# Kernel optimization log

Measured on AMD Instinct MI355X. Metric: run time of the kernel, lower is better.

Reference implementation:

```python
import jax, jax.numpy as jnp
import numpy as np

N = 50000      # nodes
E = 800000     # edges (avg degree 16)
RAW = 128      # raw_dim
HID = 256      # hidden_dim
OUT = 64       # out_dim
K = 4          # n_kernels
PHI = 16       # phi_dim
EPS = 1e-8


def setup_inputs() -> dict:
    key = jax.random.key(0)
    ks = jax.random.split(key, 8)
    h_l = jax.random.normal(ks[0], (N, HID), jnp.float32)
    e_l = jax.random.normal(ks[1], (N, RAW), jnp.float32)
    src = jax.random.randint(ks[2], (E,), 0, N, dtype=jnp.int32)
    dst = jax.random.randint(ks[3], (E,), 0, N, dtype=jnp.int32)
    gain = np.sqrt(2.0)
    W_phi = jax.random.normal(ks[4], (RAW, PHI - 1), jnp.float32) * (gain * np.sqrt(2.0 / (RAW + PHI - 1)))
    W1 = jax.random.normal(ks[5], (HID, RAW), jnp.float32) * np.sqrt(2.0 / (RAW + HID))
    b1 = jnp.zeros((HID,), jnp.float32)
    W2 = jax.random.normal(ks[6], (K * PHI, HID), jnp.float32) * np.sqrt(2.0 / (HID + K * PHI))
    b2 = jnp.zeros((K * PHI,), jnp.float32)
    tilde_phi = jnp.eye(PHI, dtype=jnp.float32)[-K:]       # n_kernels <= phi_dim branch
    W = jax.random.normal(ks[7], (HID, OUT * K), jnp.float32) * (gain * np.sqrt(2.0 / (HID + OUT * K)))
    bias = jnp.zeros((OUT,), jnp.float32)
    return {"h_l": h_l, "e_l": e_l, "src": src, "dst": dst,
            "W_phi": W_phi, "W1": W1, "b1": b1, "W2": W2, "b2": b2,
            "tilde_phi": tilde_phi, "W": W, "bias": bias}


def reference(h_l, e_l, src, dst, W_phi, W1, b1, W2, b2, tilde_phi, W, bias):
    # per-node kernelized features: [N, K, OUT]
    h = (h_l @ W).reshape(N, K, OUT)
    # pseudo-coordinates: [N, PHI-1]
    phi_k = e_l @ W_phi
    # normalized kernel anchors: [K, PHI]
    tilde_norm = tilde_phi / jnp.linalg.norm(tilde_phi, axis=1, keepdims=True)
    # deformation offsets: [N, K, PHI]
    hid = jax.nn.relu(e_l @ W1.T + b1)
    delta_k = (hid @ W2.T + b2).reshape(N, K, PHI)
    delta_ik = tilde_norm[None, :, :] + delta_k            # [N, K, PHI]

    # edge relative position (u_sub_v): [E, PHI-1]
    dist = phi_k[src] - phi_k[dst]
    mask = jnp.all(dist == 0.0, axis=1)                    # self/coincident edges
    dist = jnp.concatenate([dist, mask.astype(dist.dtype)[:, None]], axis=1)  # [E, PHI]
    dist = dist / jnp.clip(jnp.linalg.norm(dist, axis=1, keepdims=True), EPS)

    # per-edge per-kernel attention logit: a_ijk = <dist, delta_ik[dst]>  -> [E, K]
    a = jnp.einsum('ep,ekp->ek', dist, delta_ik[dst])

    # edge_softmax: softmax over incoming edges per destination node
    m = jax.ops.segment_max(a, dst, num_segments=N)        # [N, K]
    ex = jnp.exp(a - m[dst])
    s = jax.ops.segment_sum(ex, dst, num_segments=N)       # [N, K]
    att = ex / s[dst]                                      # [E, K]

    # message passing: u_mul_e then sum over incoming edges
    msg = h[src] * att[:, :, None]                         # [E, K, OUT]
    agg = jax.ops.segment_sum(msg, dst, num_segments=N)    # [N, K, OUT]

    out = agg.sum(axis=1) + bias[None, :]                  # [N, OUT]
    out = out / jnp.clip(jnp.linalg.norm(out, axis=1, keepdims=True), EPS)

    # regularizers
    d2 = ((tilde_norm[:, None, :] - tilde_norm[None, :, :]) ** 2).sum(-1)  # [K, K]
    l_sep = d2.sum() / K                                   # sum_k mean_j ||.||^2
    l_focus = (delta_k ** 2).sum(-1).mean()
    return out, l_sep, l_focus
```

## Files before the change

### kernel.cpp

```cpp
#include <hip/hip_runtime.h>
#include <math.h>

#define NN 50000
#define EE 800000

typedef __attribute__((ext_vector_type(8))) short short8;
typedef __attribute__((ext_vector_type(4))) float f32x4;
typedef __attribute__((ext_vector_type(2))) float f32x2;

__device__ inline unsigned short f2b(float f) {
    unsigned u = __float_as_uint(f);
    unsigned r = (u + 0x7FFFu + ((u >> 16) & 1u)) >> 16;
    return (unsigned short)r;
}
__device__ inline unsigned char f2fp8(float v) {
    return (unsigned char)(__builtin_amdgcn_cvt_pk_fp8_f32(v, v, 0, false) & 0xFF);
}
__device__ inline unsigned cvt_pk_bf16(float lo, float hi) {
    unsigned r;
    asm("v_cvt_pk_bf16_f32 %0, %1, %2" : "=v"(r) : "v"(lo), "v"(hi));
    return r;
}
__device__ inline void gload16(const unsigned short* g, unsigned short* l) {
    __builtin_amdgcn_global_load_lds(
        (const __attribute__((address_space(1))) void*)g,
        (__attribute__((address_space(3))) void*)l, 16, 0, 0);
}

#define PREP_THREADS (800000 + 65536 + 32768 + 16384 + 2048)

__global__ __launch_bounds__(256) void prep_k(const float* __restrict__ W,
                                              const float* __restrict__ W1,
                                              const float* __restrict__ W2,
                                              const float* __restrict__ W_phi,
                                              const float* __restrict__ tilde_phi,
                                              const int* __restrict__ dst,
                                              unsigned short* __restrict__ W_t,
                                              unsigned short* __restrict__ W1_bf,
                                              unsigned short* __restrict__ W2_bf,
                                              unsigned short* __restrict__ Wphi_t,
                                              int* __restrict__ deg,
                                              int* __restrict__ rank,
                                              float* __restrict__ tnorm,
                                              float* __restrict__ lsep_out) {
    if (blockIdx.x == 0) {
        __shared__ float tn[64];
        int t = threadIdx.x;
        if (t < 64) {
            float v = tilde_phi[t];
            float sq = v * v;
            #pragma unroll
            for (int s = 8; s; s >>= 1) sq += __shfl_xor(sq, s, 16);
            float tnv = v / sqrtf(sq);
            tn[t] = tnv;
            tnorm[t] = tnv;
        }
        __syncthreads();
        if (t == 0) {
            float tot = 0.f;
            for (int a = 0; a < 4; ++a)
                for (int b = 0; b < 4; ++b) {
                    float s2 = 0.f;
                    for (int p = 0; p < 16; ++p) {
                        float df = tn[a * 16 + p] - tn[b * 16 + p];
                        s2 += df * df;
                    }
                    tot += s2;
                }
            lsep_out[0] = tot * 0.25f;
        }
    }
    int i = blockIdx.x * 256 + threadIdx.x;
    if (i < 800000) {
        rank[i] = atomicAdd(&deg[dst[i]], 1);
    } else if (i < 865536) {
        int j = i - 800000;
        int cp = j >> 8, r = j & 255;
        int ch = cp >> 2, k = cp & 3;
        W_t[j] = f2b(W[(size_t)r * 256 + (k << 6) + ch]);
    } else if (i < 898304) {
        int j = i - 865536;
        W1_bf[j] = f2b(W1[j]);
    } else if (i < 914688) {
        int j = i - 898304;
        W2_bf[j] = f2b(W2[j]);
    } else if (i < 916736) {
        int j = i - 914688;
        int cp = j >> 7, r = j & 127;
        Wphi_t[j] = (cp < 15) ? f2b(W_phi[(size_t)r * 15 + cp]) : (unsigned short)0;
    }
}

template <int KD, int BM, int BN, int WR, int WC, bool RELU, int OMODE,
          bool AF32, bool LFOCUS, bool TNADJ>
__device__ __forceinline__ void ggemm_body(unsigned short* lds,
                                           const void* __restrict__ A,
                                           const unsigned short* __restrict__ Bt,
                                           const float* __restrict__ bias_vec,
                                           void* __restrict__ Cout, int ldc,
                                           float* __restrict__ lfocus_part,
                                           const float* __restrict__ tn_vec,
                                           int bxm, int bxn) {
    const int AM = BM / (WR * 16), AN = BN / (WC * 16);
    unsigned short* As = lds;
    unsigned short* Bs = lds + BM * 32;
    const int tid = threadIdx.x;
    const int l = tid & 63, l15 = l & 15, l4 = l >> 4;
    const int w = tid >> 6;
    const int wr = w / WC, wc = w % WC;
    const int row0 = bxm * BM;
    const int col0 = bxn * BN;
    const int wrow = wr * AM * 16, wcol = wc * AN * 16;

    auto stage = [&](int k0) {
        #pragma unroll
        for (int o = tid; o < BM * 4; o += 256) {
            int r = o >> 2, s = o & 3;
            int gr = row0 + r; if (gr >= NN) gr = NN - 1;
            if (AF32) {
                const float* Af = (const float*)A + (size_t)gr * KD + k0 + s * 8;
                float4 f0 = *(const float4*)Af;
                float4 f1 = *(const float4*)(Af + 4);
                *(uint4*)&As[o * 8] = make_uint4(cvt_pk_bf16(f0.x, f0.y),
                                                 cvt_pk_bf16(f0.z, f0.w),
                                                 cvt_pk_bf16(f1.x, f1.y),
                                                 cvt_pk_bf16(f1.z, f1.w));
            } else {
                gload16(&((const unsigned short*)A)[(size_t)gr * KD + k0 + s * 8],
                        &As[(o - l) * 8]);
            }
        }
        #pragma unroll
        for (int o = tid; o < BN * 4; o += 256) {
            int r = o >> 2, s = o & 3;
            gload16(&Bt[(size_t)(col0 + r) * KD + k0 + s * 8], &Bs[(o - l) * 8]);
        }
    };

    f32x4 acc[AM][AN];
    #pragma unroll
    for (int m = 0; m < AM; ++m)
        #pragma unroll
        for (int n = 0; n < AN; ++n)
            acc[m][n] = (f32x4){0.f, 0.f, 0.f, 0.f};

    const int NT = KD / 32;
    stage(0);
    for (int t = 0; t < NT; ++t) {
        __syncthreads();
        short8 af[AM], bfr[AN];
        #pragma unroll
        for (int m = 0; m < AM; ++m)
            af[m] = *(const short8*)&As[((wrow + m * 16 + l15) * 4 + l4) * 8];
        #pragma unroll
        for (int n = 0; n < AN; ++n)
            bfr[n] = *(const short8*)&Bs[((wcol + n * 16 + l15) * 4 + l4) * 8];
        #pragma unroll
        for (int m = 0; m < AM; ++m)
            #pragma unroll
            for (int n = 0; n < AN; ++n)
                acc[m][n] = __builtin_amdgcn_mfma_f32_16x16x32_bf16(af[m], bfr[n], acc[m][n], 0, 0, 0);
        if (t + 1 < NT) {
            __syncthreads();
            stage((t + 1) * 32);
        }
    }

    float lf = 0.f;
    #pragma unroll
    for (int m = 0; m < AM; ++m) {
        #pragma unroll
        for (int n = 0; n < AN; ++n) {
            int gc = col0 + wcol + n * 16 + l15;
            float bv = bias_vec ? bias_vec[gc] : 0.f;
            float tv = TNADJ ? tn_vec[gc] : 0.f;
            #pragma unroll
            for (int r = 0; r < 4; ++r) {
                int gr = row0 + wrow + m * 16 + l4 * 4 + r;
                if (gr >= NN) continue;
                float v = acc[m][n][r] + bv;
                if (RELU) v = fmaxf(v, 0.f);
                if (LFOCUS) lf += v * v;
                if (TNADJ) v += tv;
                if (OMODE == 0)
                    ((float*)Cout)[(size_t)gr * ldc + gc] = v;
                else if (OMODE == 1)
                    ((unsigned short*)Cout)[(size_t)gr * ldc + gc] = f2b(v);
                else
                    ((unsigned char*)Cout)[(size_t)gr * ldc + gc] = f2fp8(v);
            }
        }
    }
    if (LFOCUS) {
        #pragma unroll
        for (int s = 32; s; s >>= 1) lf += __shfl_xor(lf, s);
        __syncthreads();
        float* red = (float*)lds;
        if (l == 0) red[w] = lf;
        __syncthreads();
        if (tid == 0)
            lfocus_part[bxm] = red[0] + red[1] + red[2] + red[3];
    }
}

__global__ __launch_bounds__(256) void fused3_k(const float* __restrict__ e_l,
                                                const float* __restrict__ h_l,
                                                const unsigned short* __restrict__ W1_bf,
                                                const unsigned short* __restrict__ Wphi_t,
                                                const unsigned short* __restrict__ W_t,
                                                const float* __restrict__ b1,
                                                unsigned short* __restrict__ hid_bf,
                                                float* __restrict__ phi,
                                                unsigned char* __restrict__ h8,
                                                const int* __restrict__ src,
                                                const int* __restrict__ dst,
                                                const int* __restrict__ rank,
                                                const int* __restrict__ offs,
                                                int* __restrict__ csr_src) {
    __shared__ __align__(16) unsigned short lds[128 * 32 + 128 * 32];
    int bx = blockIdx.x;
    if (bx < 391) {
        int base = bx * 2048 + threadIdx.x;
        int pos[8], sv[8];
        #pragma unroll
        for (int j = 0; j < 8; ++j) {
            int e = base + j * 256;
            if (e < EE) {
                pos[j] = offs[dst[e]] + rank[e];
                sv[j] = src[e];
            } else pos[j] = -1;
        }
        #pragma unroll
        for (int j = 0; j < 8; ++j)
            if (pos[j] >= 0) csr_src[pos[j]] = sv[j];
    } else if (bx < 1173) {
        int b = bx - 391;
        ggemm_body<256, 128, 128, 2, 2, false, 2, true, false, false>(
            lds, h_l, W_t, nullptr, h8, 256, nullptr, nullptr, b >> 1, b & 1);
    } else if (bx < 1955) {
        int b = bx - 1173;
        ggemm_body<128, 128, 128, 2, 2, true, 1, true, false, false>(
            lds, e_l, W1_bf, b1, hid_bf, 256, nullptr, nullptr, b >> 1, b & 1);
    } else {
        ggemm_body<128, 128, 16, 4, 1, false, 0, true, false, false>(
            lds, e_l, Wphi_t, nullptr, phi, 16, nullptr, nullptr, bx - 1955, 0);
    }
}

__global__ __launch_bounds__(256) void delta_k(const unsigned short* __restrict__ hid_bf,
                                               const unsigned short* __restrict__ W2_bf,
                                               const float* __restrict__ b2,
                                               float* __restrict__ deltap,
                                               float* __restrict__ lfocus_part,
                                               const float* __restrict__ tnorm) {
    __shared__ __align__(16) unsigned short lds[32 * 32 + 64 * 32];
    ggemm_body<256, 32, 64, 1, 4, false, 0, false, true, true>(
        lds, hid_bf, W2_bf, b2, deltap, 64, lfocus_part, tnorm, blockIdx.x, 0);
}

#define SCAN_NB ((NN + 255) / 256)
#define DELTA_NB 1563

__global__ __launch_bounds__(256) void scan_partial_k(const int* __restrict__ deg,
                                                      int* __restrict__ bsum) {
    __shared__ int ws_[4];
    int i = blockIdx.x * 256 + threadIdx.x;
    int v = (i < NN) ? deg[i] : 0;
    int x = v;
    #pragma unroll
    for (int s = 32; s; s >>= 1) x += __shfl_xor(x, s);
    if ((threadIdx.x & 63) == 0) ws_[threadIdx.x >> 6] = x;
    __syncthreads();
    if (threadIdx.x == 0) bsum[blockIdx.x] = ws_[0] + ws_[1] + ws_[2] + ws_[3];
}

__global__ __launch_bounds__(256) void scan_bsum_k(int* __restrict__ bsum) {
    __shared__ int sd[256];
    int t = threadIdx.x;
    int v = (t < SCAN_NB) ? bsum[t] : 0;
    sd[t] = v;
    __syncthreads();
    for (int s = 1; s < 256; s <<= 1) {
        int u = (t >= s) ? sd[t - s] : 0;
        __syncthreads();
        sd[t] += u;
        __syncthreads();
    }
    if (t < SCAN_NB) bsum[t] = sd[t] - v;
}

__global__ __launch_bounds__(256) void scan_scatter_k(const int* __restrict__ deg,
                                                      const int* __restrict__ bsum,
                                                      int* __restrict__ offs,
                                                      int* __restrict__ csr_dst) {
    __shared__ int wexc[4];
    int i = blockIdx.x * 256 + threadIdx.x;
    int lane = threadIdx.x & 63, wid = threadIdx.x >> 6;
    int v = (i < NN) ? deg[i] : 0;
    int x = v;
    #pragma unroll
    for (int d = 1; d < 64; d <<= 1) { int u = __shfl_up(x, d); if (lane >= d) x += u; }
    if (lane == 63) wexc[wid] = x;
    __syncthreads();
    if (threadIdx.x == 0) {
        int a = wexc[0], b = wexc[1], c = wexc[2];
        wexc[0] = 0; wexc[1] = a; wexc[2] = a + b; wexc[3] = a + b + c;
    }
    __syncthreads();
    int excl = (x - v) + wexc[wid] + bsum[blockIdx.x];
    if (i < NN) {
        offs[i + 1] = excl + v;
        if (i == 0) offs[0] = 0;
        for (int q = excl; q < excl + v; ++q) csr_dst[q] = i;
    }
}

__global__ __launch_bounds__(256) void edge_w_k(const int* __restrict__ csr_src,
                                                const int* __restrict__ csr_dst,
                                                const float* __restrict__ phi,
                                                const float* __restrict__ deltap,
                                                float4* __restrict__ csr_w,
                                                const float* __restrict__ lfocus_part,
                                                float* __restrict__ lfocus_out) {
    if (blockIdx.x == 3125) {
        __shared__ float red[4];
        float s = 0.f;
        for (int i = threadIdx.x; i < DELTA_NB; i += 256) s += lfocus_part[i];
        #pragma unroll
        for (int st = 32; st; st >>= 1) s += __shfl_xor(s, st);
        if ((threadIdx.x & 63) == 0) red[threadIdx.x >> 6] = s;
        __syncthreads();
        if (threadIdx.x == 0)
            lfocus_out[0] = (red[0] + red[1] + red[2] + red[3]) * (1.f / ((float)NN * 4));
        return;
    }
    int e = blockIdx.x * 256 + threadIdx.x;
    if (e >= EE) return;
    int s = csr_src[e], d = csr_dst[e];
    const float4* ps4 = (const float4*)(phi + (size_t)s * 16);
    const float4* pd4 = (const float4*)(phi + (size_t)d * 16);
    float dv[16];
    float nrm2 = 0.f;
    #pragma unroll
    for (int q = 0; q < 4; ++q) {
        float4 a = ps4[q], b = pd4[q];
        dv[q * 4 + 0] = a.x - b.x;
        dv[q * 4 + 1] = a.y - b.y;
        dv[q * 4 + 2] = a.z - b.z;
        dv[q * 4 + 3] = a.w - b.w;
    }
    #pragma unroll
    for (int p = 0; p < 15; ++p) nrm2 += dv[p] * dv[p];
    float z = (nrm2 == 0.f) ? 1.f : 0.f;
    dv[15] = z;
    nrm2 += z;
    float inv = 1.f / fmaxf(sqrtf(nrm2), 1e-8f);
    const float* dl = deltap + (size_t)d * 64;
    float res[4];
    #pragma unroll
    for (int k = 0; k < 4; ++k) {
        const float4* dk = (const float4*)(dl + k * 16);
        float sacc = 0.f;
        #pragma unroll
        for (int q = 0; q < 4; ++q) {
            float4 tv = dk[q];
            sacc += dv[q * 4 + 0] * tv.x;
            sacc += dv[q * 4 + 1] * tv.y;
            sacc += dv[q * 4 + 2] * tv.z;
            sacc += dv[q * 4 + 3] * tv.w;
        }
        res[k] = sacc * inv;
    }
    csr_w[e] = make_float4(__expf(res[0]), __expf(res[1]),
                           __expf(res[2]), __expf(res[3]));
}

__global__ __launch_bounds__(256) void aggregate_k(const int* __restrict__ offs,
                                                   const int* __restrict__ csr_src,
                                                   const float* __restrict__ csr_wf,
                                                   const unsigned int* __restrict__ h8,
                                                   const float* __restrict__ bias,
                                                   float* __restrict__ out) {
    int wave = threadIdx.x >> 6;
    int lane = threadIdx.x & 63;
    int n = blockIdx.x * 4 + wave;
    if (n >= NN) return;
    int beg = offs[n], end = offs[n + 1];

    float part = 0.f;
    for (int q = beg * 4 + lane; q < end * 4; q += 64) part += csr_wf[q];
    #pragma unroll
    for (int s = 4; s < 64; s <<= 1) part += __shfl_xor(part, s);
    float inv = (part > 0.f) ? 1.f / part : 0.f;
    float i0 = __shfl(inv, 0), i1 = __shfl(inv, 1);
    float i2 = __shfl(inv, 2), i3 = __shfl(inv, 3);

    const float4* csr_w = (const float4*)csr_wf;
    float a0 = 0.f, a1 = 0.f, a2 = 0.f, a3 = 0.f;
    int p = beg;
    for (; p + 3 < end; p += 4) {
        float4 w0 = csr_w[p], w1 = csr_w[p + 1], w2 = csr_w[p + 2], w3 = csr_w[p + 3];
        int s0 = csr_src[p], s1 = csr_src[p + 1], s2 = csr_src[p + 2], s3 = csr_src[p + 3];
        unsigned hv0 = h8[(size_t)s0 * 64 + lane];
        unsigned hv1 = h8[(size_t)s1 * 64 + lane];
        unsigned hv2 = h8[(size_t)s2 * 64 + lane];
        unsigned hv3 = h8[(size_t)s3 * 64 + lane];
        f32x2 lo, hi;
        lo = __builtin_amdgcn_cvt_pk_f32_fp8(hv0, false);
        hi = __builtin_amdgcn_cvt_pk_f32_fp8(hv0, true);
        a0 += w0.x * lo.x; a1 += w0.y * lo.y; a2 += w0.z * hi.x; a3 += w0.w * hi.y;
        lo = __builtin_amdgcn_cvt_pk_f32_fp8(hv1, false);
        hi = __builtin_amdgcn_cvt_pk_f32_fp8(hv1, true);
        a0 += w1.x * lo.x; a1 += w1.y * lo.y; a2 += w1.z * hi.x; a3 += w1.w * hi.y;
        lo = __builtin_amdgcn_cvt_pk_f32_fp8(hv2, false);
        hi = __builtin_amdgcn_cvt_pk_f32_fp8(hv2, true);
        a0 += w2.x * lo.x; a1 += w2.y * lo.y; a2 += w2.z * hi.x; a3 += w2.w * hi.y;
        lo = __builtin_amdgcn_cvt_pk_f32_fp8(hv3, false);
        hi = __builtin_amdgcn_cvt_pk_f32_fp8(hv3, true);
        a0 += w3.x * lo.x; a1 += w3.y * lo.y; a2 += w3.z * hi.x; a3 += w3.w * hi.y;
    }
    for (; p < end; ++p) {
        float4 wA = csr_w[p];
        int sA = csr_src[p];
        unsigned hv = h8[(size_t)sA * 64 + lane];
        f32x2 lo = __builtin_amdgcn_cvt_pk_f32_fp8(hv, false);
        f32x2 hi = __builtin_amdgcn_cvt_pk_f32_fp8(hv, true);
        a0 += wA.x * lo.x; a1 += wA.y * lo.y; a2 += wA.z * hi.x; a3 += wA.w * hi.y;
    }
    float v = a0 * i0 + a1 * i1 + a2 * i2 + a3 * i3 + bias[lane];
    float nr = v * v;
    #pragma unroll
    for (int s = 32; s; s >>= 1) nr += __shfl_xor(nr, s);
    float invn = 1.f / fmaxf(sqrtf(nr), 1e-8f);
    out[(size_t)n * 64 + lane] = v * invn;
}

extern "C" void kernel_launch(void* const* d_in, const int* in_sizes, int n_in,
                              void* d_out, int out_size, void* d_ws, size_t ws_size,
                              hipStream_t stream) {
    const float* h_l       = (const float*)d_in[0];
    const float* e_l       = (const float*)d_in[1];
    const int*   src       = (const int*)d_in[2];
    const int*   dst       = (const int*)d_in[3];
    const float* W_phi     = (const float*)d_in[4];
    const float* W1        = (const float*)d_in[5];
    const float* b1        = (const float*)d_in[6];
    const float* W2        = (const float*)d_in[7];
    const float* b2        = (const float*)d_in[8];
    const float* tilde_phi = (const float*)d_in[9];
    const float* W         = (const float*)d_in[10];
    const float* bias      = (const float*)d_in[11];
    float* out = (float*)d_out;
    float* lsep_ptr   = out + (size_t)NN * 64;
    float* lfocus_ptr = out + (size_t)NN * 64 + 1;

    char* ws = (char*)d_ws;
    size_t off = 0;
    auto alloc = [&](size_t bytes) -> char* {
        char* p = ws + off;
        off += (bytes + 255) & ~(size_t)255;
        return p;
    };
    float*          phi     = (float*)alloc((size_t)NN * 16 * 4);
    float*          deltap  = (float*)alloc((size_t)NN * 64 * 4);
    unsigned char*  h8      = (unsigned char*)alloc((size_t)NN * 256);
    unsigned short* hid_bf  = (unsigned short*)alloc((size_t)NN * 256 * 2);
    int*            csr_src = (int*)alloc((size_t)EE * 4);
    int*            csr_dst = (int*)alloc((size_t)EE * 4);
    int*            rank    = (int*)alloc((size_t)EE * 4);
    float*          csr_w   = (float*)alloc((size_t)EE * 4 * 4);
    int*            deg     = (int*)alloc((size_t)NN * 4);
    int*            offs    = (int*)alloc((size_t)(NN + 1) * 4);
    int*            bsum    = (int*)alloc((size_t)SCAN_NB * 4);
    float*          lf_part = (float*)alloc((size_t)DELTA_NB * 4);
    unsigned short* W_t     = (unsigned short*)alloc(256 * 256 * 2);
    unsigned short* W1_bf   = (unsigned short*)alloc(256 * 128 * 2);
    unsigned short* W2_bf   = (unsigned short*)alloc(64 * 256 * 2);
    unsigned short* Wphi_t  = (unsigned short*)alloc(16 * 128 * 2);
    float*          tnorm   = (float*)alloc(64 * 4);

    hipMemsetAsync(deg, 0, (size_t)NN * 4, stream);

    prep_k<<<(PREP_THREADS + 255) / 256, 256, 0, stream>>>(
        W, W1, W2, W_phi, tilde_phi, dst,
        W_t, W1_bf, W2_bf, Wphi_t, deg, rank, tnorm, lsep_ptr);

    scan_partial_k<<<SCAN_NB, 256, 0, stream>>>(deg, bsum);
    scan_bsum_k<<<1, 256, 0, stream>>>(bsum);
    scan_scatter_k<<<SCAN_NB, 256, 0, stream>>>(deg, bsum, offs, csr_dst);

    fused3_k<<<2346, 256, 0, stream>>>(e_l, h_l, W1_bf, Wphi_t, W_t, b1,
                                       hid_bf, phi, h8, src, dst, rank, offs,
                                       csr_src);

    delta_k<<<DELTA_NB, 256, 0, stream>>>(hid_bf, W2_bf, b2, deltap, lf_part, tnorm);

    edge_w_k<<<3126, 256, 0, stream>>>(csr_src, csr_dst, phi, deltap, (float4*)csr_w,
                                       lf_part, lfocus_ptr);

    aggregate_k<<<12500, 256, 0, stream>>>(offs, csr_src, csr_w,
                                           (const unsigned int*)h8, bias, out);
}
```

Before: 178.9 us.

## Fuse hidden-layer GEMM, phi projection and delta GEMM into one block

The W1 GEMM, the W_phi projection and the W2 delta GEMM now run inside one fused block per 64-row tile. The ReLU hidden activations stay in padded LDS instead of being written to a global bf16 buffer and read back by a separate kernel. This removes the hidden-activation global round trip and one kernel launch, and the fused kernel moves to 512-thread blocks. In exchange it uses more LDS per block and gives the hidden and delta stage fewer, heavier blocks, which can lower occupancy.

```diff
diff --git a/kernel.cpp b/kernel.cpp
--- a/kernel.cpp
+++ b/kernel.cpp
@@ -91,175 +91,241 @@
     }
 }
 
-template <int KD, int BM, int BN, int WR, int WC, bool RELU, int OMODE,
-          bool AF32, bool LFOCUS, bool TNADJ>
-__device__ __forceinline__ void ggemm_body(unsigned short* lds,
-                                           const void* __restrict__ A,
-                                           const unsigned short* __restrict__ Bt,
-                                           const float* __restrict__ bias_vec,
-                                           void* __restrict__ Cout, int ldc,
-                                           float* __restrict__ lfocus_part,
-                                           const float* __restrict__ tn_vec,
-                                           int bxm, int bxn) {
-    const int AM = BM / (WR * 16), AN = BN / (WC * 16);
+__device__ __forceinline__ void hgemm8_body(unsigned short* lds,
+                                            const float* __restrict__ A,
+                                            const unsigned short* __restrict__ Bt,
+                                            unsigned char* __restrict__ h8,
+                                            int bxm, int bxn) {
     unsigned short* As = lds;
-    unsigned short* Bs = lds + BM * 32;
+    unsigned short* Bs = lds + 4096;
     const int tid = threadIdx.x;
     const int l = tid & 63, l15 = l & 15, l4 = l >> 4;
     const int w = tid >> 6;
-    const int wr = w / WC, wc = w % WC;
-    const int row0 = bxm * BM;
-    const int col0 = bxn * BN;
-    const int wrow = wr * AM * 16, wcol = wc * AN * 16;
+    const int wr = w >> 1, wc = w & 1;
+    const int row0 = bxm * 128, col0 = bxn * 128;
+    const int wrow = wr * 32, wcol = wc * 64;
 
     auto stage = [&](int k0) {
-        #pragma unroll
-        for (int o = tid; o < BM * 4; o += 256) {
-            int r = o >> 2, s = o & 3;
+        {
+            int o = tid, r = o >> 2, s = o & 3;
             int gr = row0 + r; if (gr >= NN) gr = NN - 1;
-            if (AF32) {
-                const float* Af = (const float*)A + (size_t)gr * KD + k0 + s * 8;
-                float4 f0 = *(const float4*)Af;
-                float4 f1 = *(const float4*)(Af + 4);
-                *(uint4*)&As[o * 8] = make_uint4(cvt_pk_bf16(f0.x, f0.y),
-                                                 cvt_pk_bf16(f0.z, f0.w),
-                                                 cvt_pk_bf16(f1.x, f1.y),
-                                                 cvt_pk_bf16(f1.z, f1.w));
-            } else {
-                gload16(&((const unsigned short*)A)[(size_t)gr * KD + k0 + s * 8],
-                        &As[(o - l) * 8]);
-            }
-        }
-        #pragma unroll
-        for (int o = tid; o < BN * 4; o += 256) {
-            int r = o >> 2, s = o & 3;
-            gload16(&Bt[(size_t)(col0 + r) * KD + k0 + s * 8], &Bs[(o - l) * 8]);
+            const float* Af = A + (size_t)gr * 256 + k0 + s * 8;
+            float4 f0 = *(const float4*)Af, f1 = *(const float4*)(Af + 4);
+            *(uint4*)&As[o * 8] = make_uint4(cvt_pk_bf16(f0.x, f0.y), cvt_pk_bf16(f0.z, f0.w),
+                                             cvt_pk_bf16(f1.x, f1.y), cvt_pk_bf16(f1.z, f1.w));
+        }
+        {
+            int o = tid, r = o >> 2, s = o & 3;
+            gload16(&Bt[(size_t)(col0 + r) * 256 + k0 + s * 8], &Bs[(o - l) * 8]);
         }
     };
 
-    f32x4 acc[AM][AN];
-    #pragma unroll
-    for (int m = 0; m < AM; ++m)
-        #pragma unroll
-        for (int n = 0; n < AN; ++n)
-            acc[m][n] = (f32x4){0.f, 0.f, 0.f, 0.f};
-
-    const int NT = KD / 32;
+    f32x4 acc[2][4];
+    #pragma unroll
+    for (int m = 0; m < 2; ++m)
+        #pragma unroll
+        for (int n = 0; n < 4; ++n) acc[m][n] = (f32x4){0.f, 0.f, 0.f, 0.f};
+
     stage(0);
-    for (int t = 0; t < NT; ++t) {
+    for (int t = 0; t < 8; ++t) {
         __syncthreads();
-        short8 af[AM], bfr[AN];
-        #pragma unroll
-        for (int m = 0; m < AM; ++m)
+        short8 af[2], bfr[4];
+        #pragma unroll
+        for (int m = 0; m < 2; ++m)
             af[m] = *(const short8*)&As[((wrow + m * 16 + l15) * 4 + l4) * 8];
         #pragma unroll
-        for (int n = 0; n < AN; ++n)
+        for (int n = 0; n < 4; ++n)
             bfr[n] = *(const short8*)&Bs[((wcol + n * 16 + l15) * 4 + l4) * 8];
         #pragma unroll
-        for (int m = 0; m < AM; ++m)
+        for (int m = 0; m < 2; ++m)
             #pragma unroll
-            for (int n = 0; n < AN; ++n)
+            for (int n = 0; n < 4; ++n)
                 acc[m][n] = __builtin_amdgcn_mfma_f32_16x16x32_bf16(af[m], bfr[n], acc[m][n], 0, 0, 0);
-        if (t + 1 < NT) {
-            __syncthreads();
-            stage((t + 1) * 32);
-        }
-    }
-
-    float lf = 0.f;
-    #pragma unroll
-    for (int m = 0; m < AM; ++m) {
-        #pragma unroll
-        for (int n = 0; n < AN; ++n) {
+        if (t + 1 < 8) { __syncthreads(); stage((t + 1) * 32); }
+    }
+    #pragma unroll
+    for (int m = 0; m < 2; ++m)
+        #pragma unroll
+        for (int n = 0; n < 4; ++n) {
             int gc = col0 + wcol + n * 16 + l15;
-            float bv = bias_vec ? bias_vec[gc] : 0.f;
-            float tv = TNADJ ? tn_vec[gc] : 0.f;
             #pragma unroll
             for (int r = 0; r < 4; ++r) {
                 int gr = row0 + wrow + m * 16 + l4 * 4 + r;
-                if (gr >= NN) continue;
-                float v = acc[m][n][r] + bv;
-                if (RELU) v = fmaxf(v, 0.f);
-                if (LFOCUS) lf += v * v;
-                if (TNADJ) v += tv;
-                if (OMODE == 0)
-                    ((float*)Cout)[(size_t)gr * ldc + gc] = v;
-                else if (OMODE == 1)
-                    ((unsigned short*)Cout)[(size_t)gr * ldc + gc] = f2b(v);
-                else
-                    ((unsigned char*)Cout)[(size_t)gr * ldc + gc] = f2fp8(v);
+                if (gr < NN) h8[(size_t)gr * 256 + gc] = f2fp8(acc[m][n][r]);
             }
         }
-    }
-    if (LFOCUS) {
-        #pragma unroll
-        for (int s = 32; s; s >>= 1) lf += __shfl_xor(lf, s);
+}
+
+#define LDPAD 264
+
+__device__ __forceinline__ void hiddelta_body(unsigned short* lds,
+                                              const float* __restrict__ e_l,
+                                              const unsigned short* __restrict__ W1_bf,
+                                              const unsigned short* __restrict__ Wphi_t,
+                                              const unsigned short* __restrict__ W2_bf,
+                                              const float* __restrict__ b1,
+                                              const float* __restrict__ b2,
+                                              const float* __restrict__ tnorm,
+                                              float* __restrict__ phi,
+                                              float* __restrict__ deltap,
+                                              float* __restrict__ lf_part, int bxm) {
+    unsigned short* As = lds;
+    unsigned short* Bs = lds + 2048;
+    unsigned short* Wp = lds + 10240;
+    unsigned short* hidL = lds;
+    const int tid = threadIdx.x;
+    const int l = tid & 63, l15 = l & 15, l4 = l >> 4;
+    const int w = tid >> 6;
+    const int wr = w >> 1, wc = w & 1;
+    const int row0 = bxm * 64;
+
+    if (tid < 256) gload16(&Wphi_t[tid * 8], &Wp[(tid - l) * 8]);
+
+    auto stage = [&](int k0) {
+        if (tid < 256) {
+            int o = tid, r = o >> 2, s = o & 3;
+            int gr = row0 + r; if (gr >= NN) gr = NN - 1;
+            const float* Af = e_l + (size_t)gr * 128 + k0 + s * 8;
+            float4 f0 = *(const float4*)Af, f1 = *(const float4*)(Af + 4);
+            *(uint4*)&As[o * 8] = make_uint4(cvt_pk_bf16(f0.x, f0.y), cvt_pk_bf16(f0.z, f0.w),
+                                             cvt_pk_bf16(f1.x, f1.y), cvt_pk_bf16(f1.z, f1.w));
+        }
+        #pragma unroll
+        for (int o = tid; o < 1024; o += 512) {
+            int r = o >> 2, s = o & 3;
+            gload16(&W1_bf[(size_t)r * 128 + k0 + s * 8], &Bs[(o - l) * 8]);
+        }
+    };
+
+    f32x4 acc[8], pacc;
+    #pragma unroll
+    for (int n = 0; n < 8; ++n) acc[n] = (f32x4){0.f, 0.f, 0.f, 0.f};
+    pacc = (f32x4){0.f, 0.f, 0.f, 0.f};
+
+    stage(0);
+    for (int t = 0; t < 4; ++t) {
+        int k0 = t * 32;
         __syncthreads();
-        float* red = (float*)lds;
-        if (l == 0) red[w] = lf;
-        __syncthreads();
-        if (tid == 0)
-            lfocus_part[bxm] = red[0] + red[1] + red[2] + red[3];
-    }
-}
-
-__global__ __launch_bounds__(256) void fused3_k(const float* __restrict__ e_l,
+        short8 af = *(const short8*)&As[((wr * 16 + l15) * 4 + l4) * 8];
+        short8 bfr[8];
+        #pragma unroll
+        for (int n = 0; n < 8; ++n)
+            bfr[n] = *(const short8*)&Bs[((wc * 128 + n * 16 + l15) * 4 + l4) * 8];
+        #pragma unroll
+        for (int n = 0; n < 8; ++n)
+            acc[n] = __builtin_amdgcn_mfma_f32_16x16x32_bf16(af, bfr[n], acc[n], 0, 0, 0);
+        if (wc == 1) {
+            short8 pf = *(const short8*)&Wp[l15 * 128 + k0 + l4 * 8];
+            pacc = __builtin_amdgcn_mfma_f32_16x16x32_bf16(af, pf, pacc, 0, 0, 0);
+        }
+        if (t + 1 < 4) { __syncthreads(); stage((t + 1) * 32); }
+    }
+
+    __syncthreads();
+    #pragma unroll
+    for (int n = 0; n < 8; ++n) {
+        int col = wc * 128 + n * 16 + l15;
+        float bv = b1[col];
+        #pragma unroll
+        for (int r = 0; r < 4; ++r) {
+            int row = wr * 16 + l4 * 4 + r;
+            hidL[row * LDPAD + col] = f2b(fmaxf(acc[n][r] + bv, 0.f));
+        }
+    }
+    if (wc == 1) {
+        #pragma unroll
+        for (int r = 0; r < 4; ++r) {
+            int gr = row0 + wr * 16 + l4 * 4 + r;
+            if (gr < NN) phi[(size_t)gr * 16 + l15] = pacc[r];
+        }
+    }
+    __syncthreads();
+
+    f32x4 acc2[2];
+    acc2[0] = (f32x4){0.f, 0.f, 0.f, 0.f};
+    acc2[1] = (f32x4){0.f, 0.f, 0.f, 0.f};
+    for (int kk = 0; kk < 8; ++kk) {
+        int k0 = kk * 32;
+        short8 a2 = *(const short8*)&hidL[(wr * 16 + l15) * LDPAD + k0 + l4 * 8];
+        #pragma unroll
+        for (int n = 0; n < 2; ++n) {
+            int col = wc * 32 + n * 16 + l15;
+            short8 b2f_ = *(const short8*)&W2_bf[(size_t)col * 256 + k0 + l4 * 8];
+            acc2[n] = __builtin_amdgcn_mfma_f32_16x16x32_bf16(a2, b2f_, acc2[n], 0, 0, 0);
+        }
+    }
+    float lf = 0.f;
+    #pragma unroll
+    for (int n = 0; n < 2; ++n) {
+        int gc = wc * 32 + n * 16 + l15;
+        float bv = b2[gc], tv = tnorm[gc];
+        #pragma unroll
+        for (int r = 0; r < 4; ++r) {
+            int gr = row0 + wr * 16 + l4 * 4 + r;
+            if (gr < NN) {
+                float v = acc2[n][r] + bv;
+                lf += v * v;
+                deltap[(size_t)gr * 64 + gc] = v + tv;
+            }
+        }
+    }
+    #pragma unroll
+    for (int s = 32; s; s >>= 1) lf += __shfl_xor(lf, s);
+    __syncthreads();
+    float* red = (float*)&lds[16896];
+    if (l == 0) red[w] = lf;
+    __syncthreads();
+    if (tid == 0) {
+        float t_ = 0.f;
+        #pragma unroll
+        for (int j = 0; j < 8; ++j) t_ += red[j];
+        lf_part[bxm] = t_;
+    }
+}
+
+__global__ __launch_bounds__(512) void fused3_k(const float* __restrict__ e_l,
                                                 const float* __restrict__ h_l,
                                                 const unsigned short* __restrict__ W1_bf,
                                                 const unsigned short* __restrict__ Wphi_t,
                                                 const unsigned short* __restrict__ W_t,
+                                                const unsigned short* __restrict__ W2_bf,
                                                 const float* __restrict__ b1,
-                                                unsigned short* __restrict__ hid_bf,
+                                                const float* __restrict__ b2,
+                                                const float* __restrict__ tnorm,
                                                 float* __restrict__ phi,
                                                 unsigned char* __restrict__ h8,
+                                                float* __restrict__ deltap,
+                                                float* __restrict__ lf_part,
                                                 const int* __restrict__ src,
                                                 const int* __restrict__ dst,
                                                 const int* __restrict__ rank,
                                                 const int* __restrict__ offs,
                                                 int* __restrict__ csr_src) {
-    __shared__ __align__(16) unsigned short lds[128 * 32 + 128 * 32];
+    __shared__ __align__(16) unsigned short lds[17408];
     int bx = blockIdx.x;
     if (bx < 391) {
         int base = bx * 2048 + threadIdx.x;
-        int pos[8], sv[8];
-        #pragma unroll
-        for (int j = 0; j < 8; ++j) {
-            int e = base + j * 256;
-            if (e < EE) {
-                pos[j] = offs[dst[e]] + rank[e];
-                sv[j] = src[e];
-            } else pos[j] = -1;
-        }
-        #pragma unroll
-        for (int j = 0; j < 8; ++j)
+        int pos[4], sv[4];
+        #pragma unroll
+        for (int j = 0; j < 4; ++j) {
+            int e = base + j * 512;
+            if (e < EE) { pos[j] = offs[dst[e]] + rank[e]; sv[j] = src[e]; }
+            else pos[j] = -1;
+        }
+        #pragma unroll
+        for (int j = 0; j < 4; ++j)
             if (pos[j] >= 0) csr_src[pos[j]] = sv[j];
     } else if (bx < 1173) {
         int b = bx - 391;
-        ggemm_body<256, 128, 128, 2, 2, false, 2, true, false, false>(
-            lds, h_l, W_t, nullptr, h8, 256, nullptr, nullptr, b >> 1, b & 1);
-    } else if (bx < 1955) {
-        int b = bx - 1173;
-        ggemm_body<128, 128, 128, 2, 2, true, 1, true, false, false>(
-            lds, e_l, W1_bf, b1, hid_bf, 256, nullptr, nullptr, b >> 1, b & 1);
+        hgemm8_body(lds, h_l, W_t, h8, b >> 1, b & 1);
     } else {
-        ggemm_body<128, 128, 16, 4, 1, false, 0, true, false, false>(
-            lds, e_l, Wphi_t, nullptr, phi, 16, nullptr, nullptr, bx - 1955, 0);
-    }
-}
-
-__global__ __launch_bounds__(256) void delta_k(const unsigned short* __restrict__ hid_bf,
-                                               const unsigned short* __restrict__ W2_bf,
-                                               const float* __restrict__ b2,
-                                               float* __restrict__ deltap,
-                                               float* __restrict__ lfocus_part,
-                                               const float* __restrict__ tnorm) {
-    __shared__ __align__(16) unsigned short lds[32 * 32 + 64 * 32];
-    ggemm_body<256, 32, 64, 1, 4, false, 0, false, true, true>(
-        lds, hid_bf, W2_bf, b2, deltap, 64, lfocus_part, tnorm, blockIdx.x, 0);
+        hiddelta_body(lds, e_l, W1_bf, Wphi_t, W2_bf, b1, b2, tnorm,
+                      phi, deltap, lf_part, bx - 1173);
+    }
 }
 
 #define SCAN_NB ((NN + 255) / 256)
-#define DELTA_NB 1563
+#define LF_NB 782
 
 __global__ __launch_bounds__(256) void scan_partial_k(const int* __restrict__ deg,
                                                       int* __restrict__ bsum) {
@@ -325,7 +391,7 @@
     if (blockIdx.x == 3125) {
         __shared__ float red[4];
         float s = 0.f;
-        for (int i = threadIdx.x; i < DELTA_NB; i += 256) s += lfocus_part[i];
+        for (int i = threadIdx.x; i < LF_NB; i += 256) s += lfocus_part[i];
         #pragma unroll
         for (int st = 32; st; st >>= 1) s += __shfl_xor(s, st);
         if ((threadIdx.x & 63) == 0) red[threadIdx.x >> 6] = s;
@@ -464,7 +530,6 @@
     float*          phi     = (float*)alloc((size_t)NN * 16 * 4);
     float*          deltap  = (float*)alloc((size_t)NN * 64 * 4);
     unsigned char*  h8      = (unsigned char*)alloc((size_t)NN * 256);
-    unsigned short* hid_bf  = (unsigned short*)alloc((size_t)NN * 256 * 2);
     int*            csr_src = (int*)alloc((size_t)EE * 4);
     int*            csr_dst = (int*)alloc((size_t)EE * 4);
     int*            rank    = (int*)alloc((size_t)EE * 4);
@@ -472,7 +537,7 @@
     int*            deg     = (int*)alloc((size_t)NN * 4);
     int*            offs    = (int*)alloc((size_t)(NN + 1) * 4);
     int*            bsum    = (int*)alloc((size_t)SCAN_NB * 4);
-    float*          lf_part = (float*)alloc((size_t)DELTA_NB * 4);
+    float*          lf_part = (float*)alloc((size_t)LF_NB * 4);
     unsigned short* W_t     = (unsigned short*)alloc(256 * 256 * 2);
     unsigned short* W1_bf   = (unsigned short*)alloc(256 * 128 * 2);
     unsigned short* W2_bf   = (unsigned short*)alloc(64 * 256 * 2);
@@ -489,11 +554,9 @@
     scan_bsum_k<<<1, 256, 0, stream>>>(bsum);
     scan_scatter_k<<<SCAN_NB, 256, 0, stream>>>(deg, bsum, offs, csr_dst);
 
-    fused3_k<<<2346, 256, 0, stream>>>(e_l, h_l, W1_bf, Wphi_t, W_t, b1,
-                                       hid_bf, phi, h8, src, dst, rank, offs,
-                                       csr_src);
-
-    delta_k<<<DELTA_NB, 256, 0, stream>>>(hid_bf, W2_bf, b2, deltap, lf_part, tnorm);
+    fused3_k<<<1955, 512, 0, stream>>>(e_l, h_l, W1_bf, Wphi_t, W_t, W2_bf,
+                                       b1, b2, tnorm, phi, h8, deltap, lf_part,
+                                       src, dst, rank, offs, csr_src);
 
     edge_w_k<<<3126, 256, 0, stream>>>(csr_src, csr_dst, phi, deltap, (float4*)csr_w,
                                        lf_part, lfocus_ptr);
```

Result: faster. 173.8 us (-2.8%).
